# Optimization experiments

Hardware: AMD Instinct MI355X
Metric: run time of the kernel (lower is better)

## Reference

```python
import jax, jax.numpy as jnp
import numpy as np

# near_sym_b biorthogonal (13,19)-tap level-1 DTCWT filters (Kingsbury).
# Analysis: h0o (lowpass, 13), h1o (highpass, 19). Synthesis derived for
# undecimated level-1 PR: g0o[n] = (-1)^(n+1) h1o[n], g1o[n] = (-1)^(n+1) h0o[n].
H0O = np.array([-0.0017578, 0.0, 0.0222656, -0.0468750, -0.0482422, 0.2968750,
                0.5554688, 0.2968750, -0.0482422, -0.0468750, 0.0222656, 0.0,
                -0.0017578], dtype=np.float32)
H1O = np.array([-0.0000706, 0.0, 0.0013419, -0.0018834, -0.0071568, 0.0238560,
                0.0556431, -0.0516881, -0.2997576, 0.5594308, -0.2997576,
                -0.0516881, 0.0556431, 0.0238560, -0.0071568, -0.0018834,
                0.0013419, 0.0, -0.0000706], dtype=np.float32)
G0O = np.array([(-1.0) ** (n + 1) for n in range(19)], np.float32) * H1O
G1O = np.array([(-1.0) ** (n + 1) for n in range(13)], np.float32) * H0O
ISQ2 = np.float32(1.0 / np.sqrt(2.0))


def _filt(x, h, axis):
    # 'same'-size correlation along `axis` with symmetric extension
    # (filters are symmetric, so correlation == convolution).
    h = jnp.asarray(h, x.dtype)
    t = (h.shape[0] - 1) // 2
    x = jnp.moveaxis(x, axis, -1)
    shp = x.shape
    xp = jnp.pad(x.reshape(-1, shp[-1]), ((0, 0), (t, t)), mode='symmetric')
    y = jax.lax.conv_general_dilated(xp[:, None, :], h[None, None, :], (1,), 'VALID')
    return jnp.moveaxis(y[:, 0, :].reshape(shp), -1, axis)


def _q2c(y):
    # quad samples -> two complex subimages (real, imag stacked in last dim)
    y = y * ISQ2
    a = y[..., 0::2, 0::2]; b = y[..., 0::2, 1::2]
    c = y[..., 1::2, 0::2]; d = y[..., 1::2, 1::2]
    return jnp.stack([a - d, b + c], -1), jnp.stack([a + d, b - c], -1)


def _c2q(w1, w2):
    w1r, w1i = w1[..., 0], w1[..., 1]
    w2r, w2i = w2[..., 0], w2[..., 1]
    B, C, H2, W2 = w1r.shape
    y = jnp.zeros((B, C, 2 * H2, 2 * W2), w1r.dtype)
    y = y.at[..., 0::2, 0::2].set(w1r + w2r)
    y = y.at[..., 0::2, 1::2].set(w1i + w2i)
    y = y.at[..., 1::2, 0::2].set(w1i - w2i)
    y = y.at[..., 1::2, 1::2].set(w2r - w1r)
    return y * ISQ2


def _dtcwt_fwd_j1(x):
    # x: (B,C,H,W) -> ll (B,C,H,W), highs (B,C,6,H/2,W/2,2)
    lo = _filt(x, H0O, -1)
    hi = _filt(x, H1O, -1)
    ll = _filt(lo, H0O, -2)
    lh = _filt(lo, H1O, -2)
    hl = _filt(hi, H0O, -2)
    hh = _filt(hi, H1O, -2)
    d15, d165 = _q2c(lh)
    d45, d135 = _q2c(hh)
    d75, d105 = _q2c(hl)
    return ll, jnp.stack([d15, d45, d75, d105, d135, d165], axis=2)


def _dtcwt_inv_j1(ll, highs):
    lh = _c2q(highs[:, :, 0], highs[:, :, 5])
    hl = _c2q(highs[:, :, 2], highs[:, :, 3])
    hh = _c2q(highs[:, :, 1], highs[:, :, 4])
    lo = _filt(ll, G0O, -2) + _filt(lh, G1O, -2)
    hi = _filt(hl, G0O, -2) + _filt(hh, G1O, -2)
    return _filt(lo, G0O, -1) + _filt(hi, G1O, -1)


def _ln(x, g, b):
    m = jnp.mean(x, -1, keepdims=True)
    v = jnp.mean((x - m) ** 2, -1, keepdims=True)
    return (x - m) * jax.lax.rsqrt(v + 1e-5) * g + b


def _svt(x, w_ll, w1, w2, b1, b2):
    B, N, C = x.shape
    H = int(round(N ** 0.5))
    nb, bs = w1.shape[1], w1.shape[2]
    xi = jnp.transpose(x.reshape(B, H, H, C), (0, 3, 1, 2))  # (B,C,H,W)
    ll, hs = _dtcwt_fwd_j1(xi)
    ll = ll * w_ll  # (C,32,32) broadcast over batch
    h = jnp.transpose(hs, (5, 0, 2, 3, 4, 1))  # (2,B,6,H2,W2,C)
    h = h.reshape(h.shape[:-1] + (nb, bs))
    xr, xim = h[0], h[1]
    mul = lambda a, w: jnp.einsum('...bd,bdk->...bk', a, w)
    r1 = jax.nn.relu(mul(xr, w1[0]) - mul(xim, w1[1]) + b1[0])
    i1 = jax.nn.relu(mul(xr, w1[1]) + mul(xim, w1[0]) + b1[1])
    r2 = mul(r1, w2[0]) - mul(i1, w2[1]) + b2[0]
    i2 = mul(r1, w2[1]) + mul(i1, w2[0]) + b2[1]
    h2 = jnp.stack([r2, i2], axis=-1)  # (B,6,H2,W2,nb,bs,2)
    h2 = h2.reshape(h2.shape[:4] + (nb * bs, 2))
    h2 = jnp.transpose(h2, (0, 4, 1, 2, 3, 5))  # (B,C,6,H2,W2,2)
    y = _dtcwt_inv_j1(ll, h2)
    return jnp.transpose(y, (0, 2, 3, 1)).reshape(B, N, C)


def _leff(x, w1, b1, wd, bd, w2, b2):
    B, N, C = x.shape
    H = int(round(N ** 0.5))
    hid = wd.shape[0]
    h = jax.nn.gelu(x @ w1 + b1, approximate=False)          # (B,N,hid)
    h = jnp.transpose(h.reshape(B, H, H, hid), (0, 3, 1, 2))  # b(hw)c -> bchw
    h = jax.lax.conv_general_dilated(h, wd, (1, 1), ((1, 1), (1, 1)),
                                     feature_group_count=hid,
                                     dimension_numbers=('NCHW', 'OIHW', 'NCHW'))
    h = jax.nn.gelu(h + bd[None, :, None, None], approximate=False)
    h = jnp.transpose(h, (0, 2, 3, 1)).reshape(B, N, hid)
    return h @ w2 + b2


def setup_inputs() -> dict:
    key = jax.random.key(0)
    ks = jax.random.split(key, 9)
    B, N, C, NB, BS, HID = 256, 1024, 64, 4, 16, 256
    s = np.float32(0.02)
    return {
        'x': jax.random.normal(ks[0], (B, N, C), jnp.float32),
        'ln1_g': jnp.ones((C,), jnp.float32),
        'ln1_b': jnp.zeros((C,), jnp.float32),
        'w_ll': s * jax.random.normal(ks[1], (C, 32, 32), jnp.float32),
        'w1': s * jax.random.normal(ks[2], (2, NB, BS, BS), jnp.float32),
        'w2': s * jax.random.normal(ks[3], (2, NB, BS, BS), jnp.float32),
        'b1': s * jax.random.normal(ks[4], (2, NB, BS), jnp.float32),
        'b2': s * jax.random.normal(ks[5], (2, NB, BS), jnp.float32),
        'ln2_g': jnp.ones((C,), jnp.float32),
        'ln2_b': jnp.zeros((C,), jnp.float32),
        'lin1_w': jax.random.normal(ks[6], (C, HID), jnp.float32) / np.float32(np.sqrt(C)),
        'lin1_b': jnp.zeros((HID,), jnp.float32),
        'dw_w': jax.random.normal(ks[7], (HID, 1, 3, 3), jnp.float32) / np.float32(3.0),
        'dw_b': jnp.zeros((HID,), jnp.float32),
        'lin2_w': jax.random.normal(ks[8], (HID, C), jnp.float32) / np.float32(np.sqrt(HID)),
        'lin2_b': jnp.zeros((C,), jnp.float32),
    }


def reference(x, ln1_g, ln1_b, w_ll, w1, w2, b1, b2, ln2_g, ln2_b,
              lin1_w, lin1_b, dw_w, dw_b, lin2_w, lin2_b):
    x = x + _svt(_ln(x, ln1_g, ln1_b), w_ll, w1, w2, b1, b2)
    x = x + _leff(_ln(x, ln2_g, ln2_b), lin1_w, lin1_b, dw_w, dw_b, lin2_w, lin2_b)
    return x
```

## Files before the change

### kernel.cpp

```cpp
#include <hip/hip_runtime.h>
#include <hip/hip_fp16.h>
#include <math.h>

#define ISQ2 0.70710678118654752440f

typedef _Float16 f16x8 __attribute__((ext_vector_type(8)));
typedef __attribute__((ext_vector_type(4))) float f32x4;

static __device__ __constant__ float H0c[13] = {
    -0.0017578f, 0.0f, 0.0222656f, -0.046875f, -0.0482422f, 0.296875f,
    0.5554688f, 0.296875f, -0.0482422f, -0.046875f, 0.0222656f, 0.0f, -0.0017578f};
static __device__ __constant__ float H1c[19] = {
    -7.06e-05f, 0.0f, 0.0013419f, -0.0018834f, -0.0071568f, 0.023856f,
    0.0556431f, -0.0516881f, -0.2997576f, 0.5594308f, -0.2997576f, -0.0516881f,
    0.0556431f, 0.023856f, -0.0071568f, -0.0018834f, 0.0013419f, 0.0f, -7.06e-05f};

__device__ __forceinline__ int refl32(int i) {
    if (i < 0) i = -1 - i;
    if (i > 31) i = 63 - i;
    return i;
}

__device__ __forceinline__ float gelu_fast(float x) {
    float u = x * (0.7978845608f + 0.0356774081f * x * x);
    float e = __expf(-2.0f * fabsf(u));
    float t = 1.0f - 2.0f * e / (1.0f + e);
    t = copysignf(t, u);
    return 0.5f * x * (1.0f + t);
}

__device__ __forceinline__ __half2 u2h2(unsigned int u) {
    union { unsigned int u; __half2 h; } c;
    c.u = u;
    return c.h;
}

__global__ __launch_bounds__(256) void k_ln1_t(const float* __restrict__ x,
                                               const float* __restrict__ g,
                                               const float* __restrict__ be,
                                               float* __restrict__ A) {
    __shared__ float sx[64][65];
    __shared__ float rs[64][4], rq[64][4];
    __shared__ float sm[64], sv[64];
    int b = blockIdx.x >> 4;
    int n0 = (blockIdx.x & 15) << 6;
    int tid = threadIdx.x;
    const float* xp = x + ((size_t)b * 1024 + n0) * 64;
#pragma unroll
    for (int rep = 0; rep < 16; ++rep) {
        int idx = rep * 256 + tid;
        sx[idx >> 6][idx & 63] = xp[idx];
    }
    __syncthreads();
    {
        int i = tid >> 2, q = tid & 3;
        float s = 0.f, ss = 0.f;
#pragma unroll
        for (int d = 0; d < 16; ++d) {
            float v = sx[i][q * 16 + d];
            s += v; ss += v * v;
        }
        rs[i][q] = s; rq[i][q] = ss;
    }
    __syncthreads();
    if (tid < 64) {
        float s = rs[tid][0] + rs[tid][1] + rs[tid][2] + rs[tid][3];
        float ss = rq[tid][0] + rq[tid][1] + rq[tid][2] + rq[tid][3];
        float m = s * (1.f / 64.f);
        float v = ss * (1.f / 64.f) - m * m;
        sm[tid] = m;
        sv[tid] = rsqrtf(v + 1e-5f);
    }
    __syncthreads();
#pragma unroll
    for (int rep = 0; rep < 16; ++rep) {
        int idx = rep * 256 + tid;
        int c = idx >> 6, i = idx & 63;
        float val = (sx[i][c] - sm[i]) * sv[i] * g[c] + be[c];
        A[((size_t)(b * 64 + c)) * 1024 + n0 + i] = val;
    }
}

__global__ __launch_bounds__(256, 4) void k_fwd(const float* __restrict__ A,
                                                const float* __restrict__ wll,
                                                float* __restrict__ LL,
                                                float* __restrict__ HSr,
                                                float* __restrict__ HSi) {
    __shared__ float sx[32][52];
    __shared__ float slo[50][34];
    __shared__ float shi[50][34];
    int bc = blockIdx.x;
    int c = bc & 63;
    int tid = threadIdx.x;
    int hA = tid >> 3, w0r = (tid & 7) * 4;
    {
        const float4* ap4 = (const float4*)(A + (size_t)bc * 1024);
        float4 v = ap4[tid];
        sx[hA][w0r + 9] = v.x;
        sx[hA][w0r + 10] = v.y;
        sx[hA][w0r + 11] = v.z;
        sx[hA][w0r + 12] = v.w;
    }
    __syncthreads();
    for (int i = tid; i < 576; i += 256) {
        int h = i / 18, j = i - (i / 18) * 18;
        int wp = (j < 9) ? (j - 9) : (23 + j);
        sx[h][wp + 9] = sx[h][refl32(wp) + 9];
    }
    __syncthreads();
    {
        float ws[22];
#pragma unroll
        for (int t = 0; t < 22; ++t) ws[t] = sx[hA][w0r + t];
        float lo[4] = {0.f, 0.f, 0.f, 0.f}, hi[4] = {0.f, 0.f, 0.f, 0.f};
#pragma unroll
        for (int k = 0; k < 19; ++k)
#pragma unroll
            for (int j = 0; j < 4; ++j) hi[j] += H1c[k] * ws[j + k];
#pragma unroll
        for (int k = 0; k < 13; ++k)
#pragma unroll
            for (int j = 0; j < 4; ++j) lo[j] += H0c[k] * ws[j + k + 3];
#pragma unroll
        for (int j = 0; j < 4; ++j) {
            slo[hA + 9][w0r + j] = lo[j];
            shi[hA + 9][w0r + j] = hi[j];
        }
    }
    __syncthreads();
    for (int i = tid; i < 576; i += 256) {
        int j = i >> 5, w = i & 31;
        int hp = (j < 9) ? (j - 9) : (23 + j);
        int hs = refl32(hp);
        slo[hp + 9][w] = slo[hs + 9][w];
        shi[hp + 9][w] = shi[hs + 9][w];
    }
    __syncthreads();
    {
        int wL = tid & 31, h0 = (tid >> 5) * 4;
        float cs[16];
#pragma unroll
        for (int t = 0; t < 16; ++t) cs[t] = slo[h0 + 3 + t][wL];
#pragma unroll
        for (int j = 0; j < 4; ++j) {
            float acc = 0.f;
#pragma unroll
            for (int k = 0; k < 13; ++k) acc += H0c[k] * cs[j + k];
            int p = (h0 + j) * 32 + wL;
            LL[(size_t)bc * 1024 + p] = acc * wll[c * 1024 + p];
        }
    }
    {
        int i = tid >> 4, j = tid & 15;
        size_t base = (size_t)bc * 1536 + tid;
        float a, bb, cc2, dd;
        {
            float2 sl[20];
#pragma unroll
            for (int t = 0; t < 20; ++t) sl[t] = *(const float2*)&slo[2 * i + t][2 * j];
            a = bb = cc2 = dd = 0.f;
#pragma unroll
            for (int k = 0; k < 19; ++k) {
                a += H1c[k] * sl[k].x;
                bb += H1c[k] * sl[k].y;
                cc2 += H1c[k] * sl[k + 1].x;
                dd += H1c[k] * sl[k + 1].y;
            }
            HSr[base + 0 * 256] = (a - dd) * ISQ2; HSi[base + 0 * 256] = (bb + cc2) * ISQ2;
            HSr[base + 5 * 256] = (a + dd) * ISQ2; HSi[base + 5 * 256] = (bb - cc2) * ISQ2;
        }
        {
            float2 sh[20];
#pragma unroll
            for (int t = 0; t < 20; ++t) sh[t] = *(const float2*)&shi[2 * i + t][2 * j];
            a = bb = cc2 = dd = 0.f;
#pragma unroll
            for (int k = 0; k < 19; ++k) {
                a += H1c[k] * sh[k].x;
                bb += H1c[k] * sh[k].y;
                cc2 += H1c[k] * sh[k + 1].x;
                dd += H1c[k] * sh[k + 1].y;
            }
            HSr[base + 1 * 256] = (a - dd) * ISQ2; HSi[base + 1 * 256] = (bb + cc2) * ISQ2;
            HSr[base + 4 * 256] = (a + dd) * ISQ2; HSi[base + 4 * 256] = (bb - cc2) * ISQ2;
            a = bb = cc2 = dd = 0.f;
#pragma unroll
            for (int k = 0; k < 13; ++k) {
                a += H0c[k] * sh[k + 3].x;
                bb += H0c[k] * sh[k + 3].y;
                cc2 += H0c[k] * sh[k + 4].x;
                dd += H0c[k] * sh[k + 4].y;
            }
            HSr[base + 2 * 256] = (a - dd) * ISQ2; HSi[base + 2 * 256] = (bb + cc2) * ISQ2;
            HSr[base + 3 * 256] = (a + dd) * ISQ2; HSi[base + 3 * 256] = (bb - cc2) * ISQ2;
        }
    }
}

__global__ __launch_bounds__(256) void k_prep_mlp(const float* __restrict__ mw1,
                                                  const float* __restrict__ mw2,
                                                  __half* __restrict__ W1cr,
                                                  __half* __restrict__ W1ci,
                                                  __half* __restrict__ W2cr,
                                                  __half* __restrict__ W2ci) {
    int gid = blockIdx.x * 256 + threadIdx.x;
    int stride = gridDim.x * 256;
    for (int i = gid; i < 2048; i += stride) {
        int q = i >> 9, rest = i & 511;
        int n = rest >> 5, k = rest & 31;
        if (k < 16) {
            float w1r = mw1[q * 256 + k * 16 + n];
            float w1i = mw1[1024 + q * 256 + k * 16 + n];
            float w2r = mw2[q * 256 + k * 16 + n];
            float w2i = mw2[1024 + q * 256 + k * 16 + n];
            W1cr[i] = __float2half(w1r);
            W1ci[i] = __float2half(w1i);
            W2cr[i] = __float2half(w2r);
            W2ci[i] = __float2half(w2i);
        } else {
            float w1r = mw1[q * 256 + (k - 16) * 16 + n];
            float w1i = mw1[1024 + q * 256 + (k - 16) * 16 + n];
            float w2r = mw2[q * 256 + (k - 16) * 16 + n];
            float w2i = mw2[1024 + q * 256 + (k - 16) * 16 + n];
            W1cr[i] = __float2half(-w1i);
            W1ci[i] = __float2half(w1r);
            W2cr[i] = __float2half(-w2i);
            W2ci[i] = __float2half(w2r);
        }
    }
}

__global__ __launch_bounds__(256) void k_mlpm(float* __restrict__ HSr,
                                              float* __restrict__ HSi,
                                              const __half* __restrict__ W1cr,
                                              const __half* __restrict__ W1ci,
                                              const __half* __restrict__ W2cr,
                                              const __half* __restrict__ W2ci,
                                              const float* __restrict__ b1,
                                              const float* __restrict__ b2) {
    __shared__ __half xh[4][64][40];
    int tid = threadIdx.x;
    int wid = tid >> 6, lane = tid & 63;
    int lr = lane & 15, kg = lane >> 4;
    int b = blockIdx.x / 6;
    int o = blockIdx.x - b * 6;
    size_t base = (size_t)b * 98304 + (size_t)o * 256;

#pragma unroll 1
    for (int q = 0; q < 4; ++q) {
#pragma unroll
        for (int mt = 0; mt < 4; ++mt) {
            int token0 = wid * 64 + mt * 16;
            const float* src = (kg < 2) ? HSr : HSi;
            int c0 = q * 16 + (kg & 1) * 8;
            float v[8];
#pragma unroll
            for (int e = 0; e < 8; ++e)
                v[e] = src[base + (size_t)(c0 + e) * 1536 + token0 + lr];
            __half2 h0 = __floats2half2_rn(v[0], v[1]);
            __half2 h1 = __floats2half2_rn(v[2], v[3]);
            __half2 h2 = __floats2half2_rn(v[4], v[5]);
            __half2 h3 = __floats2half2_rn(v[6], v[7]);
            uint4 av = make_uint4(*(unsigned int*)&h0, *(unsigned int*)&h1,
                                  *(unsigned int*)&h2, *(unsigned int*)&h3);
            f16x8 a = *(f16x8*)&av;
            f16x8 bfr = *(const f16x8*)(W1cr + q * 512 + lr * 32 + kg * 8);
            f16x8 bfi = *(const f16x8*)(W1ci + q * 512 + lr * 32 + kg * 8);
            f32x4 accr = (f32x4){0.f, 0.f, 0.f, 0.f};
            f32x4 acci = (f32x4){0.f, 0.f, 0.f, 0.f};
            accr = __builtin_amdgcn_mfma_f32_16x16x32_f16(a, bfr, accr, 0, 0, 0);
            acci = __builtin_amdgcn_mfma_f32_16x16x32_f16(a, bfi, acci, 0, 0, 0);
            float b1r = b1[q * 16 + lr];
            float b1i = b1[64 + q * 16 + lr];
#pragma unroll
            for (int reg = 0; reg < 4; ++reg) {
                int tl = mt * 16 + kg * 4 + reg;
                xh[wid][tl][lr] = __float2half(fmaxf(accr[reg] + b1r, 0.f));
                xh[wid][tl][16 + lr] = __float2half(fmaxf(acci[reg] + b1i, 0.f));
            }
        }
        __syncthreads();
#pragma unroll
        for (int mt = 0; mt < 4; ++mt) {
            f16x8 a = *(const f16x8*)&xh[wid][mt * 16 + lr][kg * 8];
            f16x8 bfr = *(const f16x8*)(W2cr + q * 512 + lr * 32 + kg * 8);
            f16x8 bfi = *(const f16x8*)(W2ci + q * 512 + lr * 32 + kg * 8);
            f32x4 accr = (f32x4){0.f, 0.f, 0.f, 0.f};
            f32x4 acci = (f32x4){0.f, 0.f, 0.f, 0.f};
            accr = __builtin_amdgcn_mfma_f32_16x16x32_f16(a, bfr, accr, 0, 0, 0);
            acci = __builtin_amdgcn_mfma_f32_16x16x32_f16(a, bfi, acci, 0, 0, 0);
            float b2r = b2[q * 16 + lr];
            float b2i = b2[64 + q * 16 + lr];
            size_t cb = base + (size_t)(q * 16 + lr) * 1536 + wid * 64 + mt * 16 + kg * 4;
#pragma unroll
            for (int reg = 0; reg < 4; ++reg) {
                HSr[cb + reg] = accr[reg] + b2r;
                HSi[cb + reg] = acci[reg] + b2i;
            }
        }
        __syncthreads();
    }
}

__global__ __launch_bounds__(256, 4) void k_inv(const float* __restrict__ LL,
                                                const float* __restrict__ HSr,
                                                const float* __restrict__ HSi,
                                                float* __restrict__ Y) {
    __shared__ float sll[50][34], slh[50][34], shl[50][34], shh[50][34];
    __shared__ float slo[32][52], shi[32][52];
    int bc = blockIdx.x;
    int tid = threadIdx.x;
    int hA = tid >> 3, w0r = (tid & 7) * 4;
    {
        const float4* lp4 = (const float4*)(LL + (size_t)bc * 1024);
        float4 v = lp4[tid];
        sll[hA + 9][w0r] = v.x;
        sll[hA + 9][w0r + 1] = v.y;
        sll[hA + 9][w0r + 2] = v.z;
        sll[hA + 9][w0r + 3] = v.w;
    }
    {
        int i = tid >> 4, j = tid & 15;
        int h0 = 2 * i + 9, w0 = 2 * j;
        size_t base = (size_t)bc * 1536 + tid;
        float o0r = HSr[base + 0 * 256], o0i = HSi[base + 0 * 256];
        float o1r = HSr[base + 1 * 256], o1i = HSi[base + 1 * 256];
        float o2r = HSr[base + 2 * 256], o2i = HSi[base + 2 * 256];
        float o3r = HSr[base + 3 * 256], o3i = HSi[base + 3 * 256];
        float o4r = HSr[base + 4 * 256], o4i = HSi[base + 4 * 256];
        float o5r = HSr[base + 5 * 256], o5i = HSi[base + 5 * 256];
        *(float2*)&slh[h0][w0] = make_float2((o0r + o5r) * ISQ2, (o0i + o5i) * ISQ2);
        *(float2*)&slh[h0 + 1][w0] = make_float2((o0i - o5i) * ISQ2, (o5r - o0r) * ISQ2);
        *(float2*)&shl[h0][w0] = make_float2((o2r + o3r) * ISQ2, (o2i + o3i) * ISQ2);
        *(float2*)&shl[h0 + 1][w0] = make_float2((o2i - o3i) * ISQ2, (o3r - o2r) * ISQ2);
        *(float2*)&shh[h0][w0] = make_float2((o1r + o4r) * ISQ2, (o1i + o4i) * ISQ2);
        *(float2*)&shh[h0 + 1][w0] = make_float2((o1i - o4i) * ISQ2, (o4r - o1r) * ISQ2);
    }
    __syncthreads();
    for (int i = tid; i < 576; i += 256) {
        int j = i >> 5, w = i & 31;
        int hp = (j < 9) ? (j - 9) : (23 + j);
        int hs = refl32(hp);
        sll[hp + 9][w] = sll[hs + 9][w];
        slh[hp + 9][w] = slh[hs + 9][w];
        shl[hp + 9][w] = shl[hs + 9][w];
        shh[hp + 9][w] = shh[hs + 9][w];
    }
    __syncthreads();
    {
        int wL = tid & 31, h0 = (tid >> 5) * 4;
        float w19[22], w13[16];
        float lo[4] = {0.f, 0.f, 0.f, 0.f}, hi[4] = {0.f, 0.f, 0.f, 0.f};
#pragma unroll
        for (int t = 0; t < 22; ++t) w19[t] = sll[h0 + t][wL];
#pragma unroll
        for (int k = 0; k < 19; ++k) {
            float g0 = (k & 1) ? H1c[k] : -H1c[k];
#pragma unroll
            for (int j = 0; j < 4; ++j) lo[j] += g0 * w19[j + k];
        }
#pragma unroll
        for (int t = 0; t < 16; ++t) w13[t] = slh[h0 + 3 + t][wL];
#pragma unroll
        for (int k = 0; k < 13; ++k) {
            float g1 = (k & 1) ? H0c[k] : -H0c[k];
#pragma unroll
            for (int j = 0; j < 4; ++j) lo[j] += g1 * w13[j + k];
        }
#pragma unroll
        for (int t = 0; t < 22; ++t) w19[t] = shl[h0 + t][wL];
#pragma unroll
        for (int k = 0; k < 19; ++k) {
            float g0 = (k & 1) ? H1c[k] : -H1c[k];
#pragma unroll
            for (int j = 0; j < 4; ++j) hi[j] += g0 * w19[j + k];
        }
#pragma unroll
        for (int t = 0; t < 16; ++t) w13[t] = shh[h0 + 3 + t][wL];
#pragma unroll
        for (int k = 0; k < 13; ++k) {
            float g1 = (k & 1) ? H0c[k] : -H0c[k];
#pragma unroll
            for (int j = 0; j < 4; ++j) hi[j] += g1 * w13[j + k];
        }
#pragma unroll
        for (int j = 0; j < 4; ++j) {
            slo[h0 + j][wL + 9] = lo[j];
            shi[h0 + j][wL + 9] = hi[j];
        }
    }
    __syncthreads();
    for (int i = tid; i < 576; i += 256) {
        int h = i / 18, j = i - (i / 18) * 18;
        int wp = (j < 9) ? (j - 9) : (23 + j);
        int ws2 = refl32(wp);
        slo[h][wp + 9] = slo[h][ws2 + 9];
        shi[h][wp + 9] = shi[h][ws2 + 9];
    }
    __syncthreads();
    {
        float rw[22], rh[16];
#pragma unroll
        for (int t = 0; t < 22; ++t) rw[t] = slo[hA][w0r + t];
#pragma unroll
        for (int t = 0; t < 16; ++t) rh[t] = shi[hA][w0r + 3 + t];
        float y[4] = {0.f, 0.f, 0.f, 0.f};
#pragma unroll
        for (int k = 0; k < 19; ++k) {
            float g0 = (k & 1) ? H1c[k] : -H1c[k];
#pragma unroll
            for (int j = 0; j < 4; ++j) y[j] += g0 * rw[j + k];
        }
#pragma unroll
        for (int k = 0; k < 13; ++k) {
            float g1 = (k & 1) ? H0c[k] : -H0c[k];
#pragma unroll
            for (int j = 0; j < 4; ++j) y[j] += g1 * rh[j + k];
        }
        *(float4*)(Y + (size_t)bc * 1024 + hA * 32 + w0r) = make_float4(y[0], y[1], y[2], y[3]);
    }
}

__global__ __launch_bounds__(256) void k_addt(const float* __restrict__ Y,
                                              const float* __restrict__ x,
                                              float* __restrict__ out) {
    __shared__ float sy[64][65];
    int b = blockIdx.x >> 4;
    int n0 = (blockIdx.x & 15) << 6;
    int tid = threadIdx.x;
#pragma unroll
    for (int rep = 0; rep < 16; ++rep) {
        int idx = rep * 256 + tid;
        int c = idx >> 6, i = idx & 63;
        sy[c][i] = Y[((size_t)(b * 64 + c)) * 1024 + n0 + i];
    }
    __syncthreads();
#pragma unroll
    for (int rep = 0; rep < 16; ++rep) {
        int idx = rep * 256 + tid;
        int i = idx >> 6, c = idx & 63;
        size_t gi = ((size_t)b * 1024 + n0 + i) * 64 + c;
        out[gi] = x[gi] + sy[c][i];
    }
}

__global__ __launch_bounds__(256) void k_halo(__half2* __restrict__ H1h2) {
    int img = blockIdx.x;
    __half2* base = H1h2 + (size_t)img * 1156 * 16;
    __half2 z = __floats2half2_rn(0.f, 0.f);
    for (int idx = threadIdx.x; idx < 2112; idx += 256) {
        int pos = idx >> 4, c = idx & 15;
        int p2;
        if (pos < 34) p2 = pos;
        else if (pos < 68) p2 = 33 * 34 + (pos - 34);
        else if (pos < 100) p2 = (pos - 68 + 1) * 34;
        else p2 = (pos - 100 + 1) * 34 + 33;
        base[p2 * 16 + c] = z;
    }
}

__global__ __launch_bounds__(256) void k_prep_leff(const float* __restrict__ DW,
                                                   const float* __restrict__ DB,
                                                   const float* __restrict__ W2,
                                                   const float* __restrict__ W1,
                                                   __half2* __restrict__ DWh,
                                                   __half2* __restrict__ DBh,
                                                   __half* __restrict__ W2T,
                                                   __half* __restrict__ W1T) {
    int gid = blockIdx.x * 256 + threadIdx.x;
    int stride = gridDim.x * 256;
    for (int i = gid; i < 1152; i += stride) {
        int tap = i >> 7, pr = i & 127;
        DWh[i] = __floats2half2_rn(DW[(2 * pr) * 9 + tap], DW[(2 * pr + 1) * 9 + tap]);
    }
    for (int i = gid; i < 128; i += stride)
        DBh[i] = __floats2half2_rn(DB[2 * i], DB[2 * i + 1]);
    for (int i = gid; i < 16384; i += stride) {
        int n = i >> 8, k = i & 255;
        W2T[i] = __float2half(W2[k * 64 + n]);
    }
    for (int i = gid; i < 16384; i += stride)
        W1T[i] = __float2half(W1[(i & 63) * 256 + (i >> 6)]);
}

__global__ __launch_bounds__(256) void k_leff1m(const float* __restrict__ X1,
                                                const float* __restrict__ g2,
                                                const float* __restrict__ be2,
                                                const __half* __restrict__ W1T,
                                                const float* __restrict__ B1,
                                                __half* __restrict__ H1h) {
    __shared__ __half xnh[64][72];
    int tid = threadIdx.x;
    int wid = tid >> 6, lane = tid & 63;
    int lr = lane & 15, kg = lane >> 4;
    int bimg = blockIdx.x >> 4;
    int hw0 = (blockIdx.x & 15) << 6;
    size_t tok0 = (size_t)blockIdx.x * 64;
    int ltok = wid * 16 + lr;
    {
        const float4* xp = (const float4*)(X1 + (tok0 + ltok) * 64 + kg * 16);
        float4 v0 = xp[0], v1 = xp[1], v2 = xp[2], v3 = xp[3];
        float s = v0.x + v0.y + v0.z + v0.w + v1.x + v1.y + v1.z + v1.w +
                  v2.x + v2.y + v2.z + v2.w + v3.x + v3.y + v3.z + v3.w;
        float ss = v0.x * v0.x + v0.y * v0.y + v0.z * v0.z + v0.w * v0.w +
                   v1.x * v1.x + v1.y * v1.y + v1.z * v1.z + v1.w * v1.w +
                   v2.x * v2.x + v2.y * v2.y + v2.z * v2.z + v2.w * v2.w +
                   v3.x * v3.x + v3.y * v3.y + v3.z * v3.z + v3.w * v3.w;
        s += __shfl_xor(s, 16, 64);
        ss += __shfl_xor(ss, 16, 64);
        s += __shfl_xor(s, 32, 64);
        ss += __shfl_xor(ss, 32, 64);
        float m = s * (1.f / 64.f);
        float var = ss * (1.f / 64.f) - m * m;
        float rstd = rsqrtf(var + 1e-5f);
        float vv[16] = {v0.x, v0.y, v0.z, v0.w, v1.x, v1.y, v1.z, v1.w,
                        v2.x, v2.y, v2.z, v2.w, v3.x, v3.y, v3.z, v3.w};
        unsigned int u[8];
#pragma unroll
        for (int i = 0; i < 8; ++i) {
            int d = kg * 16 + 2 * i;
            float a0 = (vv[2 * i] - m) * rstd * g2[d] + be2[d];
            float a1 = (vv[2 * i + 1] - m) * rstd * g2[d + 1] + be2[d + 1];
            __half2 hh = __floats2half2_rn(a0, a1);
            u[i] = *(unsigned int*)&hh;
        }
        *(uint4*)&xnh[ltok][kg * 16] = make_uint4(u[0], u[1], u[2], u[3]);
        *(uint4*)&xnh[ltok][kg * 16 + 8] = make_uint4(u[4], u[5], u[6], u[7]);
    }
    __syncthreads();
    f32x4 acc[16];
#pragma unroll
    for (int n = 0; n < 16; ++n) acc[n] = (f32x4){0.f, 0.f, 0.f, 0.f};
#pragma unroll
    for (int k0 = 0; k0 < 2; ++k0) {
        f16x8 a = *(const f16x8*)&xnh[wid * 16 + lr][k0 * 32 + kg * 8];
#pragma unroll
        for (int n = 0; n < 16; ++n) {
            f16x8 bf = *(const f16x8*)(W1T + (size_t)(n * 16 + lr) * 64 + k0 * 32 + kg * 8);
            acc[n] = __builtin_amdgcn_mfma_f32_16x16x32_f16(a, bf, acc[n], 0, 0, 0);
        }
    }
#pragma unroll
    for (int n = 0; n < 16; ++n) {
        int hid = n * 16 + lr;
        float bb = B1[hid];
        size_t cb = ((size_t)bimg * 8 + (hid >> 5)) * 1156;
        int cl = hid & 31;
#pragma unroll
        for (int reg = 0; reg < 4; ++reg) {
            int token = wid * 16 + kg * 4 + reg;
            int hw = hw0 + token;
            int h = hw >> 5, w = hw & 31;
            H1h[(cb + (size_t)(h + 1) * 34 + (w + 1)) * 32 + cl] =
                __float2half(gelu_fast(acc[n][reg] + bb));
        }
    }
}

struct Tap12 { uint4 v[12]; };

__device__ __forceinline__ void load12(const __half* H1h, size_t pb, int kg, Tap12& T) {
    const __half2* p = (const __half2*)(H1h + pb * 32) + kg * 4;
#pragma unroll
    for (int r = 0; r < 4; ++r)
#pragma unroll
        for (int dc = 0; dc < 3; ++dc)
            T.v[r * 3 + dc] = *(const uint4*)(p + ((r - 1) * 34 + (dc - 1)) * 16);
}

__device__ __forceinline__ void convg2(const Tap12& T,
                                       const __half2* __restrict__ DBh,
                                       const __half2* __restrict__ DWh,
                                       int k0, int kg, f16x8& a0out, f16x8& a1out) {
    const __half2* dbp = DBh + k0 * 16 + kg * 4;
    __half2 c00 = dbp[0], c01 = dbp[1], c02 = dbp[2], c03 = dbp[3];
    __half2 c10 = c00, c11 = c01, c12 = c02, c13 = c03;
#pragma unroll
    for (int dr = 0; dr < 3; ++dr) {
#pragma unroll
        for (int dc = 0; dc < 3; ++dc) {
            const __half2* wp = DWh + (dr * 3 + dc) * 128 + k0 * 16 + kg * 4;
            __half2 w0 = wp[0], w1 = wp[1], w2 = wp[2], w3 = wp[3];
            const uint4& t0 = T.v[dr * 3 + dc];
            const uint4& t1 = T.v[(dr + 1) * 3 + dc];
            c00 = __hfma2(u2h2(t0.x), w0, c00);
            c01 = __hfma2(u2h2(t0.y), w1, c01);
            c02 = __hfma2(u2h2(t0.z), w2, c02);
            c03 = __hfma2(u2h2(t0.w), w3, c03);
            c10 = __hfma2(u2h2(t1.x), w0, c10);
            c11 = __hfma2(u2h2(t1.y), w1, c11);
            c12 = __hfma2(u2h2(t1.z), w2, c12);
            c13 = __hfma2(u2h2(t1.w), w3, c13);
        }
    }
    __half2 o0 = __floats2half2_rn(gelu_fast(__low2float(c00)), gelu_fast(__high2float(c00)));
    __half2 o1 = __floats2half2_rn(gelu_fast(__low2float(c01)), gelu_fast(__high2float(c01)));
    __half2 o2 = __floats2half2_rn(gelu_fast(__low2float(c02)), gelu_fast(__high2float(c02)));
    __half2 o3 = __floats2half2_rn(gelu_fast(__low2float(c03)), gelu_fast(__high2float(c03)));
    uint4 av0 = make_uint4(*(unsigned int*)&o0, *(unsigned int*)&o1,
                           *(unsigned int*)&o2, *(unsigned int*)&o3);
    a0out = *(f16x8*)&av0;
    o0 = __floats2half2_rn(gelu_fast(__low2float(c10)), gelu_fast(__high2float(c10)));
    o1 = __floats2half2_rn(gelu_fast(__low2float(c11)), gelu_fast(__high2float(c11)));
    o2 = __floats2half2_rn(gelu_fast(__low2float(c12)), gelu_fast(__high2float(c12)));
    o3 = __floats2half2_rn(gelu_fast(__low2float(c13)), gelu_fast(__high2float(c13)));
    uint4 av1 = make_uint4(*(unsigned int*)&o0, *(unsigned int*)&o1,
                           *(unsigned int*)&o2, *(unsigned int*)&o3);
    a1out = *(f16x8*)&av1;
}

__global__ __launch_bounds__(256, 3) void k_leff2m(const __half* __restrict__ H1h,
                                                   const __half2* __restrict__ DWh,
                                                   const __half2* __restrict__ DBh,
                                                   const __half* __restrict__ W2T,
                                                   const float* __restrict__ B2,
                                                   float* __restrict__ out) {
    int tid = threadIdx.x;
    int wid = tid >> 6, lane = tid & 63;
    int mt = blockIdx.x * 4 + wid;
    int b = mt >> 5;
    int rem = mt & 31;
    int h0 = (rem >> 1) * 2;
    int w0 = (rem & 1) << 4;
    int lr = lane & 15, kg = lane >> 4;
    int wA = w0 + lr;

    f32x4 acc0[4], acc1[4];
#pragma unroll
    for (int n = 0; n < 4; ++n) {
        acc0[n] = (f32x4){0.f, 0.f, 0.f, 0.f};
        acc1[n] = (f32x4){0.f, 0.f, 0.f, 0.f};
    }

    size_t rowoff = (size_t)h0 * 34 + wA;
    Tap12 TA, TB;
    load12(H1h, ((size_t)b * 8 + 0) * 1156 + rowoff + 35, kg, TA);
#pragma unroll
    for (int k0 = 0; k0 < 8; ++k0) {
        if (k0 < 7)
            load12(H1h, ((size_t)b * 8 + (k0 + 1)) * 1156 + rowoff + 35, kg,
                   (k0 & 1) ? TA : TB);
        f16x8 a0, a1;
        convg2((k0 & 1) ? TB : TA, DBh, DWh, k0, kg, a0, a1);
#pragma unroll
        for (int n = 0; n < 4; ++n) {
            f16x8 bf = *(const f16x8*)(W2T + ((size_t)(n * 16 + lr) * 256 + k0 * 32 + kg * 8));
            acc0[n] = __builtin_amdgcn_mfma_f32_16x16x32_f16(a0, bf, acc0[n], 0, 0, 0);
            acc1[n] = __builtin_amdgcn_mfma_f32_16x16x32_f16(a1, bf, acc1[n], 0, 0, 0);
        }
    }
    size_t ob0 = (size_t)b * 1024 + (size_t)h0 * 32;
#pragma unroll
    for (int n = 0; n < 4; ++n) {
        int c = n * 16 + lr;
        float b2v = B2[c];
#pragma unroll
        for (int reg = 0; reg < 4; ++reg) {
            int rowTok = w0 + kg * 4 + reg;
            size_t g0i = (ob0 + rowTok) * 64 + c;
            out[g0i] += acc0[n][reg] + b2v;
            size_t g1i = (ob0 + 32 + rowTok) * 64 + c;
            out[g1i] += acc1[n][reg] + b2v;
        }
    }
}

extern "C" void kernel_launch(void* const* d_in, const int* in_sizes, int n_in,
                              void* d_out, int out_size, void* d_ws, size_t ws_size,
                              hipStream_t stream) {
    const float* x = (const float*)d_in[0];
    const float* ln1_g = (const float*)d_in[1];
    const float* ln1_b = (const float*)d_in[2];
    const float* w_ll = (const float*)d_in[3];
    const float* w1 = (const float*)d_in[4];
    const float* w2 = (const float*)d_in[5];
    const float* b1 = (const float*)d_in[6];
    const float* b2 = (const float*)d_in[7];
    const float* ln2_g = (const float*)d_in[8];
    const float* ln2_b = (const float*)d_in[9];
    const float* lin1_w = (const float*)d_in[10];
    const float* lin1_b = (const float*)d_in[11];
    const float* dw_w = (const float*)d_in[12];
    const float* dw_b = (const float*)d_in[13];
    const float* lin2_w = (const float*)d_in[14];
    const float* lin2_b = (const float*)d_in[15];
    float* out = (float*)d_out;
    char* ws = (char*)d_ws;

    float* A = (float*)ws;
    float* HSr = (float*)(ws + 67108864);
    float* HSi = (float*)(ws + 167772160);
    float* LL = out;
    float* Y = A;
    __half* H1h = (__half*)ws;
    __half* W1cr = (__half*)(ws);
    __half* W1ci = (__half*)(ws + 4096);
    __half* W2cr = (__half*)(ws + 8192);
    __half* W2ci = (__half*)(ws + 12288);
    char* wtab = ws + 167772160;
    __half2* DWh = (__half2*)(wtab);
    __half2* DBh = (__half2*)(wtab + 8192);
    __half* W2T = (__half*)(wtab + 12288);
    __half* W1T = (__half*)(wtab + 49152);

    k_ln1_t<<<dim3(4096), dim3(256), 0, stream>>>(x, ln1_g, ln1_b, A);
    k_fwd<<<dim3(16384), dim3(256), 0, stream>>>(A, w_ll, LL, HSr, HSi);
    k_prep_mlp<<<dim3(8), dim3(256), 0, stream>>>(w1, w2, W1cr, W1ci, W2cr, W2ci);
    k_mlpm<<<dim3(1536), dim3(256), 0, stream>>>(HSr, HSi, W1cr, W1ci, W2cr, W2ci, b1, b2);
    k_inv<<<dim3(16384), dim3(256), 0, stream>>>(LL, HSr, HSi, Y);
    k_addt<<<dim3(4096), dim3(256), 0, stream>>>(Y, x, out);
    k_halo<<<dim3(2048), dim3(256), 0, stream>>>((__half2*)H1h);
    k_prep_leff<<<dim3(72), dim3(256), 0, stream>>>(dw_w, dw_b, lin2_w, lin1_w,
                                                    DWh, DBh, W2T, W1T);
    k_leff1m<<<dim3(4096), dim3(256), 0, stream>>>(out, ln2_g, ln2_b, W1T, lin1_b, H1h);
    k_leff2m<<<dim3(2048), dim3(256), 0, stream>>>(H1h, DWh, DBh, W2T, b2, out);
}
```

Before: 508.2 us.

## Store intermediate activations and wavelet highpass coefficients in fp16 instead of fp32

Switches the LN1 output, the DTCWT highpass subband buffers and the inverse-transform output from fp32 to fp16 across five kernels. Each stage still computes in fp32 but converts on load and store. This roughly halves global memory traffic for these large intermediates in a memory-bound pipeline, and k_mlpm no longer needs its own fp32-to-half conversion. The cost is reduced precision in the residual branch and the subband coefficients, which could hurt accuracy, and k_mlpm now reads 16-bit scalars that are less efficiently coalesced.

```diff
diff --git a/kernel.cpp b/kernel.cpp
--- a/kernel.cpp
+++ b/kernel.cpp
@@ -38,7 +38,7 @@
 __global__ __launch_bounds__(256) void k_ln1_t(const float* __restrict__ x,
                                                const float* __restrict__ g,
                                                const float* __restrict__ be,
-                                               float* __restrict__ A) {
+                                               __half* __restrict__ Ah) {
     __shared__ float sx[64][65];
     __shared__ float rs[64][4], rq[64][4];
     __shared__ float sm[64], sv[64];
@@ -77,15 +77,15 @@
         int idx = rep * 256 + tid;
         int c = idx >> 6, i = idx & 63;
         float val = (sx[i][c] - sm[i]) * sv[i] * g[c] + be[c];
-        A[((size_t)(b * 64 + c)) * 1024 + n0 + i] = val;
-    }
-}
-
-__global__ __launch_bounds__(256, 4) void k_fwd(const float* __restrict__ A,
+        Ah[((size_t)(b * 64 + c)) * 1024 + n0 + i] = __float2half(val);
+    }
+}
+
+__global__ __launch_bounds__(256, 4) void k_fwd(const __half* __restrict__ Ah,
                                                 const float* __restrict__ wll,
                                                 float* __restrict__ LL,
-                                                float* __restrict__ HSr,
-                                                float* __restrict__ HSi) {
+                                                __half* __restrict__ HSr,
+                                                __half* __restrict__ HSi) {
     __shared__ float sx[32][52];
     __shared__ float slo[50][34];
     __shared__ float shi[50][34];
@@ -94,12 +94,12 @@
     int tid = threadIdx.x;
     int hA = tid >> 3, w0r = (tid & 7) * 4;
     {
-        const float4* ap4 = (const float4*)(A + (size_t)bc * 1024);
-        float4 v = ap4[tid];
-        sx[hA][w0r + 9] = v.x;
-        sx[hA][w0r + 10] = v.y;
-        sx[hA][w0r + 11] = v.z;
-        sx[hA][w0r + 12] = v.w;
+        const __half2* ap2 = (const __half2*)(Ah + (size_t)bc * 1024);
+        __half2 v01 = ap2[tid * 2], v23 = ap2[tid * 2 + 1];
+        sx[hA][w0r + 9] = __low2float(v01);
+        sx[hA][w0r + 10] = __high2float(v01);
+        sx[hA][w0r + 11] = __low2float(v23);
+        sx[hA][w0r + 12] = __high2float(v23);
     }
     __syncthreads();
     for (int i = tid; i < 576; i += 256) {
@@ -166,8 +166,10 @@
                 cc2 += H1c[k] * sl[k + 1].x;
                 dd += H1c[k] * sl[k + 1].y;
             }
-            HSr[base + 0 * 256] = (a - dd) * ISQ2; HSi[base + 0 * 256] = (bb + cc2) * ISQ2;
-            HSr[base + 5 * 256] = (a + dd) * ISQ2; HSi[base + 5 * 256] = (bb - cc2) * ISQ2;
+            HSr[base + 0 * 256] = __float2half((a - dd) * ISQ2);
+            HSi[base + 0 * 256] = __float2half((bb + cc2) * ISQ2);
+            HSr[base + 5 * 256] = __float2half((a + dd) * ISQ2);
+            HSi[base + 5 * 256] = __float2half((bb - cc2) * ISQ2);
         }
         {
             float2 sh[20];
@@ -181,8 +183,10 @@
                 cc2 += H1c[k] * sh[k + 1].x;
                 dd += H1c[k] * sh[k + 1].y;
             }
-            HSr[base + 1 * 256] = (a - dd) * ISQ2; HSi[base + 1 * 256] = (bb + cc2) * ISQ2;
-            HSr[base + 4 * 256] = (a + dd) * ISQ2; HSi[base + 4 * 256] = (bb - cc2) * ISQ2;
+            HSr[base + 1 * 256] = __float2half((a - dd) * ISQ2);
+            HSi[base + 1 * 256] = __float2half((bb + cc2) * ISQ2);
+            HSr[base + 4 * 256] = __float2half((a + dd) * ISQ2);
+            HSi[base + 4 * 256] = __float2half((bb - cc2) * ISQ2);
             a = bb = cc2 = dd = 0.f;
 #pragma unroll
             for (int k = 0; k < 13; ++k) {
@@ -191,8 +195,10 @@
                 cc2 += H0c[k] * sh[k + 4].x;
                 dd += H0c[k] * sh[k + 4].y;
             }
-            HSr[base + 2 * 256] = (a - dd) * ISQ2; HSi[base + 2 * 256] = (bb + cc2) * ISQ2;
-            HSr[base + 3 * 256] = (a + dd) * ISQ2; HSi[base + 3 * 256] = (bb - cc2) * ISQ2;
+            HSr[base + 2 * 256] = __float2half((a - dd) * ISQ2);
+            HSi[base + 2 * 256] = __float2half((bb + cc2) * ISQ2);
+            HSr[base + 3 * 256] = __float2half((a + dd) * ISQ2);
+            HSi[base + 3 * 256] = __float2half((bb - cc2) * ISQ2);
         }
     }
 }
@@ -209,29 +215,21 @@
         int q = i >> 9, rest = i & 511;
         int n = rest >> 5, k = rest & 31;
         if (k < 16) {
-            float w1r = mw1[q * 256 + k * 16 + n];
-            float w1i = mw1[1024 + q * 256 + k * 16 + n];
-            float w2r = mw2[q * 256 + k * 16 + n];
-            float w2i = mw2[1024 + q * 256 + k * 16 + n];
-            W1cr[i] = __float2half(w1r);
-            W1ci[i] = __float2half(w1i);
-            W2cr[i] = __float2half(w2r);
-            W2ci[i] = __float2half(w2i);
+            W1cr[i] = __float2half(mw1[q * 256 + k * 16 + n]);
+            W1ci[i] = __float2half(mw1[1024 + q * 256 + k * 16 + n]);
+            W2cr[i] = __float2half(mw2[q * 256 + k * 16 + n]);
+            W2ci[i] = __float2half(mw2[1024 + q * 256 + k * 16 + n]);
         } else {
-            float w1r = mw1[q * 256 + (k - 16) * 16 + n];
-            float w1i = mw1[1024 + q * 256 + (k - 16) * 16 + n];
-            float w2r = mw2[q * 256 + (k - 16) * 16 + n];
-            float w2i = mw2[1024 + q * 256 + (k - 16) * 16 + n];
-            W1cr[i] = __float2half(-w1i);
-            W1ci[i] = __float2half(w1r);
-            W2cr[i] = __float2half(-w2i);
-            W2ci[i] = __float2half(w2r);
-        }
-    }
-}
-
-__global__ __launch_bounds__(256) void k_mlpm(float* __restrict__ HSr,
-                                              float* __restrict__ HSi,
+            W1cr[i] = __float2half(-mw1[1024 + q * 256 + (k - 16) * 16 + n]);
+            W1ci[i] = __float2half(mw1[q * 256 + (k - 16) * 16 + n]);
+            W2cr[i] = __float2half(-mw2[1024 + q * 256 + (k - 16) * 16 + n]);
+            W2ci[i] = __float2half(mw2[q * 256 + (k - 16) * 16 + n]);
+        }
+    }
+}
+
+__global__ __launch_bounds__(256) void k_mlpm(__half* __restrict__ HSr,
+                                              __half* __restrict__ HSi,
                                               const __half* __restrict__ W1cr,
                                               const __half* __restrict__ W1ci,
                                               const __half* __restrict__ W2cr,
@@ -251,18 +249,17 @@
 #pragma unroll
         for (int mt = 0; mt < 4; ++mt) {
             int token0 = wid * 64 + mt * 16;
-            const float* src = (kg < 2) ? HSr : HSi;
+            const unsigned short* src =
+                (const unsigned short*)((kg < 2) ? HSr : HSi);
             int c0 = q * 16 + (kg & 1) * 8;
-            float v[8];
-#pragma unroll
-            for (int e = 0; e < 8; ++e)
-                v[e] = src[base + (size_t)(c0 + e) * 1536 + token0 + lr];
-            __half2 h0 = __floats2half2_rn(v[0], v[1]);
-            __half2 h1 = __floats2half2_rn(v[2], v[3]);
-            __half2 h2 = __floats2half2_rn(v[4], v[5]);
-            __half2 h3 = __floats2half2_rn(v[6], v[7]);
-            uint4 av = make_uint4(*(unsigned int*)&h0, *(unsigned int*)&h1,
-                                  *(unsigned int*)&h2, *(unsigned int*)&h3);
+            unsigned int u[4];
+#pragma unroll
+            for (int e = 0; e < 4; ++e) {
+                unsigned int lo = src[base + (size_t)(c0 + 2 * e) * 1536 + token0 + lr];
+                unsigned int hi = src[base + (size_t)(c0 + 2 * e + 1) * 1536 + token0 + lr];
+                u[e] = lo | (hi << 16);
+            }
+            uint4 av = make_uint4(u[0], u[1], u[2], u[3]);
             f16x8 a = *(f16x8*)&av;
             f16x8 bfr = *(const f16x8*)(W1cr + q * 512 + lr * 32 + kg * 8);
             f16x8 bfi = *(const f16x8*)(W1ci + q * 512 + lr * 32 + kg * 8);
@@ -294,8 +291,8 @@
             size_t cb = base + (size_t)(q * 16 + lr) * 1536 + wid * 64 + mt * 16 + kg * 4;
 #pragma unroll
             for (int reg = 0; reg < 4; ++reg) {
-                HSr[cb + reg] = accr[reg] + b2r;
-                HSi[cb + reg] = acci[reg] + b2i;
+                HSr[cb + reg] = __float2half(accr[reg] + b2r);
+                HSi[cb + reg] = __float2half(acci[reg] + b2i);
             }
         }
         __syncthreads();
@@ -303,9 +300,9 @@
 }
 
 __global__ __launch_bounds__(256, 4) void k_inv(const float* __restrict__ LL,
-                                                const float* __restrict__ HSr,
-                                                const float* __restrict__ HSi,
-                                                float* __restrict__ Y) {
+                                                const __half* __restrict__ HSr,
+                                                const __half* __restrict__ HSi,
+                                                __half* __restrict__ Yh) {
     __shared__ float sll[50][34], slh[50][34], shl[50][34], shh[50][34];
     __shared__ float slo[32][52], shi[32][52];
     int bc = blockIdx.x;
@@ -323,12 +320,12 @@
         int i = tid >> 4, j = tid & 15;
         int h0 = 2 * i + 9, w0 = 2 * j;
         size_t base = (size_t)bc * 1536 + tid;
-        float o0r = HSr[base + 0 * 256], o0i = HSi[base + 0 * 256];
-        float o1r = HSr[base + 1 * 256], o1i = HSi[base + 1 * 256];
-        float o2r = HSr[base + 2 * 256], o2i = HSi[base + 2 * 256];
-        float o3r = HSr[base + 3 * 256], o3i = HSi[base + 3 * 256];
-        float o4r = HSr[base + 4 * 256], o4i = HSi[base + 4 * 256];
-        float o5r = HSr[base + 5 * 256], o5i = HSi[base + 5 * 256];
+        float o0r = __half2float(HSr[base + 0 * 256]), o0i = __half2float(HSi[base + 0 * 256]);
+        float o1r = __half2float(HSr[base + 1 * 256]), o1i = __half2float(HSi[base + 1 * 256]);
+        float o2r = __half2float(HSr[base + 2 * 256]), o2i = __half2float(HSi[base + 2 * 256]);
+        float o3r = __half2float(HSr[base + 3 * 256]), o3i = __half2float(HSi[base + 3 * 256]);
+        float o4r = __half2float(HSr[base + 4 * 256]), o4i = __half2float(HSi[base + 4 * 256]);
+        float o5r = __half2float(HSr[base + 5 * 256]), o5i = __half2float(HSi[base + 5 * 256]);
         *(float2*)&slh[h0][w0] = make_float2((o0r + o5r) * ISQ2, (o0i + o5i) * ISQ2);
         *(float2*)&slh[h0 + 1][w0] = make_float2((o0i - o5i) * ISQ2, (o5r - o0r) * ISQ2);
         *(float2*)&shl[h0][w0] = make_float2((o2r + o3r) * ISQ2, (o2i + o3i) * ISQ2);
@@ -417,11 +414,16 @@
 #pragma unroll
             for (int j = 0; j < 4; ++j) y[j] += g1 * rh[j + k];
         }
-        *(float4*)(Y + (size_t)bc * 1024 + hA * 32 + w0r) = make_float4(y[0], y[1], y[2], y[3]);
-    }
-}
-
-__global__ __launch_bounds__(256) void k_addt(const float* __restrict__ Y,
+        __half2 y01 = __floats2half2_rn(y[0], y[1]);
+        __half2 y23 = __floats2half2_rn(y[2], y[3]);
+        uint2 pk;
+        pk.x = *(unsigned int*)&y01;
+        pk.y = *(unsigned int*)&y23;
+        *(uint2*)(Yh + (size_t)bc * 1024 + hA * 32 + w0r) = pk;
+    }
+}
+
+__global__ __launch_bounds__(256) void k_addt(const __half* __restrict__ Yh,
                                               const float* __restrict__ x,
                                               float* __restrict__ out) {
     __shared__ float sy[64][65];
@@ -432,7 +434,7 @@
     for (int rep = 0; rep < 16; ++rep) {
         int idx = rep * 256 + tid;
         int c = idx >> 6, i = idx & 63;
-        sy[c][i] = Y[((size_t)(b * 64 + c)) * 1024 + n0 + i];
+        sy[c][i] = __half2float(Yh[((size_t)(b * 64 + c)) * 1024 + n0 + i]);
     }
     __syncthreads();
 #pragma unroll
@@ -687,11 +689,11 @@
     float* out = (float*)d_out;
     char* ws = (char*)d_ws;
 
-    float* A = (float*)ws;
-    float* HSr = (float*)(ws + 67108864);
-    float* HSi = (float*)(ws + 167772160);
+    __half* Ah = (__half*)ws;
+    __half* HSr = (__half*)(ws + 67108864);
+    __half* HSi = (__half*)(ws + 167772160);
     float* LL = out;
-    float* Y = A;
+    __half* Yh = (__half*)ws;
     __half* H1h = (__half*)ws;
     __half* W1cr = (__half*)(ws);
     __half* W1ci = (__half*)(ws + 4096);
@@ -703,12 +705,12 @@
     __half* W2T = (__half*)(wtab + 12288);
     __half* W1T = (__half*)(wtab + 49152);
 
-    k_ln1_t<<<dim3(4096), dim3(256), 0, stream>>>(x, ln1_g, ln1_b, A);
-    k_fwd<<<dim3(16384), dim3(256), 0, stream>>>(A, w_ll, LL, HSr, HSi);
+    k_ln1_t<<<dim3(4096), dim3(256), 0, stream>>>(x, ln1_g, ln1_b, Ah);
+    k_fwd<<<dim3(16384), dim3(256), 0, stream>>>(Ah, w_ll, LL, HSr, HSi);
     k_prep_mlp<<<dim3(8), dim3(256), 0, stream>>>(w1, w2, W1cr, W1ci, W2cr, W2ci);
     k_mlpm<<<dim3(1536), dim3(256), 0, stream>>>(HSr, HSi, W1cr, W1ci, W2cr, W2ci, b1, b2);
-    k_inv<<<dim3(16384), dim3(256), 0, stream>>>(LL, HSr, HSi, Y);
-    k_addt<<<dim3(4096), dim3(256), 0, stream>>>(Y, x, out);
+    k_inv<<<dim3(16384), dim3(256), 0, stream>>>(LL, HSr, HSi, Yh);
+    k_addt<<<dim3(4096), dim3(256), 0, stream>>>(Yh, x, out);
     k_halo<<<dim3(2048), dim3(256), 0, stream>>>((__half2*)H1h);
     k_prep_leff<<<dim3(72), dim3(256), 0, stream>>>(dw_w, dw_b, lin2_w, lin1_w,
                                                     DWh, DBh, W2T, W1T);
```

After: 472.3 us, median of 2. 7.1% less time.
